# Kernel tuning notes

Hardware: AMD Instinct MI355X
Metric: run time of the kernel (lower is better)

Reference implementation:

```python
import jax, jax.numpy as jnp
import numpy as np

N = 8388608  # flattened batch*seq tokens
C = 2        # binary classification, per source


def setup_inputs() -> dict:
    key = jax.random.key(0)
    k1, k2 = jax.random.split(key)
    x = jax.random.normal(k1, (N, C), dtype=jnp.float32)
    targets = jax.random.randint(k2, (N,), 0, 2, dtype=jnp.int64)
    return {"x": x, "targets": targets}


def reference(x, targets):
    # log-softmax over classes
    logs = jax.nn.log_softmax(x, axis=1)  # [N, C]
    # gather log-prob at the target class per sample
    picked = jnp.take_along_axis(logs, targets[:, None].astype(jnp.int32), axis=1)[:, 0]  # [N]
    is_one = (targets == 1)
    is_zero = (targets == 0)
    n_one = jnp.sum(is_one)
    n_zero = jnp.sum(is_zero)
    sum_one = jnp.sum(jnp.where(is_one, picked, 0.0))
    sum_zero = jnp.sum(jnp.where(is_zero, picked, 0.0))
    # class-conditional mean of -log p; 0 if the class is absent
    r = jnp.where(n_one > 0, -sum_one / jnp.maximum(n_one, 1), 0.0)
    p = jnp.where(n_zero > 0, -sum_zero / jnp.maximum(n_zero, 1), 0.0)
    return p + r
```

## Files before the change

kernel.cpp:

```cpp
#include <hip/hip_runtime.h>

#define BLOCK 256
#define NBLOCKS 2048
#define BLOCK2 256

__global__ __launch_bounds__(BLOCK) void nll_partial(
    const float4* __restrict__ x4,
    const int4* __restrict__ t4,
    float* __restrict__ ps0,
    float* __restrict__ ps1,
    unsigned int* __restrict__ pc1,
    int nquads)
{
    int idx = blockIdx.x * blockDim.x + threadIdx.x;
    int stride = gridDim.x * blockDim.x;

    float s0 = 0.f, s1 = 0.f;
    unsigned int c1 = 0;

    for (int i = idx; i < nquads; i += stride) {
        float4 xa = x4[2 * i];
        float4 xb = x4[2 * i + 1];
        int4   t  = t4[i];

        float a, b, m, lse;

        a = xa.x; b = xa.y;
        m = fmaxf(a, b);
        lse = m + __logf(__expf(a - m) + __expf(b - m));
        s1 += t.x ? (lse - b) : 0.f;
        s0 += t.x ? 0.f : (lse - a);
        c1 += (t.x != 0);

        a = xa.z; b = xa.w;
        m = fmaxf(a, b);
        lse = m + __logf(__expf(a - m) + __expf(b - m));
        s1 += t.y ? (lse - b) : 0.f;
        s0 += t.y ? 0.f : (lse - a);
        c1 += (t.y != 0);

        a = xb.x; b = xb.y;
        m = fmaxf(a, b);
        lse = m + __logf(__expf(a - m) + __expf(b - m));
        s1 += t.z ? (lse - b) : 0.f;
        s0 += t.z ? 0.f : (lse - a);
        c1 += (t.z != 0);

        a = xb.z; b = xb.w;
        m = fmaxf(a, b);
        lse = m + __logf(__expf(a - m) + __expf(b - m));
        s1 += t.w ? (lse - b) : 0.f;
        s0 += t.w ? 0.f : (lse - a);
        c1 += (t.w != 0);
    }

    for (int off = 32; off > 0; off >>= 1) {
        s0 += __shfl_down(s0, off, 64);
        s1 += __shfl_down(s1, off, 64);
        c1 += __shfl_down(c1, off, 64);
    }

    __shared__ float sh0[BLOCK / 64];
    __shared__ float sh1[BLOCK / 64];
    __shared__ unsigned int shc[BLOCK / 64];

    int lane = threadIdx.x & 63;
    int wave = threadIdx.x >> 6;
    if (lane == 0) { sh0[wave] = s0; sh1[wave] = s1; shc[wave] = c1; }
    __syncthreads();

    if (threadIdx.x == 0) {
        float t0 = 0.f, t1 = 0.f;
        unsigned int tc = 0;
        for (int w = 0; w < BLOCK / 64; ++w) { t0 += sh0[w]; t1 += sh1[w]; tc += shc[w]; }
        ps0[blockIdx.x] = t0;
        ps1[blockIdx.x] = t1;
        pc1[blockIdx.x] = tc;
    }
}

__global__ __launch_bounds__(BLOCK2) void nll_finalize(
    const float* __restrict__ ps0,
    const float* __restrict__ ps1,
    const unsigned int* __restrict__ pc1,
    const float* __restrict__ x,
    const int* __restrict__ tg,
    float* __restrict__ out,
    int P, int N, int tail_start)
{
    float s0 = 0.f, s1 = 0.f;
    unsigned int c1 = 0;
    for (int i = threadIdx.x; i < P; i += BLOCK2) {
        s0 += ps0[i];
        s1 += ps1[i];
        c1 += pc1[i];
    }

    for (int off = 32; off > 0; off >>= 1) {
        s0 += __shfl_down(s0, off, 64);
        s1 += __shfl_down(s1, off, 64);
        c1 += __shfl_down(c1, off, 64);
    }

    __shared__ float sh0[BLOCK2 / 64];
    __shared__ float sh1[BLOCK2 / 64];
    __shared__ unsigned int shc[BLOCK2 / 64];

    int lane = threadIdx.x & 63;
    int wave = threadIdx.x >> 6;
    if (lane == 0) { sh0[wave] = s0; sh1[wave] = s1; shc[wave] = c1; }
    __syncthreads();

    if (threadIdx.x == 0) {
        float t0 = 0.f, t1 = 0.f;
        unsigned int tc = 0;
        for (int w = 0; w < BLOCK2 / 64; ++w) { t0 += sh0[w]; t1 += sh1[w]; tc += shc[w]; }
        for (int i = tail_start; i < N; ++i) {
            float a = x[2 * i], b = x[2 * i + 1];
            float m = fmaxf(a, b);
            float lse = m + __logf(__expf(a - m) + __expf(b - m));
            if (tg[i]) { t1 += lse - b; tc++; } else { t0 += lse - a; }
        }
        unsigned int c0 = (unsigned int)N - tc;
        float r = (tc > 0) ? t1 / (float)tc : 0.f;
        float p = (c0 > 0) ? t0 / (float)c0 : 0.f;
        out[0] = p + r;
    }
}

__global__ void nll_atomic(const float4* __restrict__ x4,
                           const int4* __restrict__ t4,
                           float* __restrict__ wsf,
                           unsigned int* __restrict__ wsi,
                           int nquads)
{
    int idx = blockIdx.x * blockDim.x + threadIdx.x;
    int stride = gridDim.x * blockDim.x;
    float s0 = 0.f, s1 = 0.f;
    unsigned int c1 = 0;
    for (int i = idx; i < nquads; i += stride) {
        float4 xa = x4[2 * i];
        float4 xb = x4[2 * i + 1];
        int4   t  = t4[i];
        float a, b, m, lse;
        a = xa.x; b = xa.y; m = fmaxf(a, b);
        lse = m + __logf(__expf(a - m) + __expf(b - m));
        s1 += t.x ? (lse - b) : 0.f; s0 += t.x ? 0.f : (lse - a); c1 += (t.x != 0);
        a = xa.z; b = xa.w; m = fmaxf(a, b);
        lse = m + __logf(__expf(a - m) + __expf(b - m));
        s1 += t.y ? (lse - b) : 0.f; s0 += t.y ? 0.f : (lse - a); c1 += (t.y != 0);
        a = xb.x; b = xb.y; m = fmaxf(a, b);
        lse = m + __logf(__expf(a - m) + __expf(b - m));
        s1 += t.z ? (lse - b) : 0.f; s0 += t.z ? 0.f : (lse - a); c1 += (t.z != 0);
        a = xb.z; b = xb.w; m = fmaxf(a, b);
        lse = m + __logf(__expf(a - m) + __expf(b - m));
        s1 += t.w ? (lse - b) : 0.f; s0 += t.w ? 0.f : (lse - a); c1 += (t.w != 0);
    }
    for (int off = 32; off > 0; off >>= 1) {
        s0 += __shfl_down(s0, off, 64);
        s1 += __shfl_down(s1, off, 64);
        c1 += __shfl_down(c1, off, 64);
    }
    __shared__ float sh0[4]; __shared__ float sh1[4]; __shared__ unsigned int shc[4];
    int lane = threadIdx.x & 63; int wave = threadIdx.x >> 6;
    if (lane == 0) { sh0[wave] = s0; sh1[wave] = s1; shc[wave] = c1; }
    __syncthreads();
    if (threadIdx.x == 0) {
        float t0 = 0.f, t1 = 0.f; unsigned int tc = 0;
        for (int w = 0; w < 4; ++w) { t0 += sh0[w]; t1 += sh1[w]; tc += shc[w]; }
        atomicAdd(&wsf[0], t0); atomicAdd(&wsf[1], t1); atomicAdd(&wsi[0], tc);
    }
}

__global__ void nll_atomic_fin(const float* __restrict__ x,
                               const int* __restrict__ tg,
                               const float* __restrict__ wsf,
                               const unsigned int* __restrict__ wsi,
                               float* __restrict__ out,
                               int N, int tail_start)
{
    float s0 = wsf[0], s1 = wsf[1];
    unsigned int c1 = wsi[0];
    for (int i = tail_start; i < N; ++i) {
        float a = x[2 * i], b = x[2 * i + 1];
        float m = fmaxf(a, b);
        float lse = m + __logf(__expf(a - m) + __expf(b - m));
        if (tg[i]) { s1 += lse - b; c1++; } else { s0 += lse - a; }
    }
    unsigned int c0 = (unsigned int)N - c1;
    float r = (c1 > 0) ? s1 / (float)c1 : 0.f;
    float p = (c0 > 0) ? s0 / (float)c0 : 0.f;
    out[0] = p + r;
}

extern "C" void kernel_launch(void* const* d_in, const int* in_sizes, int n_in,
                              void* d_out, int out_size, void* d_ws, size_t ws_size,
                              hipStream_t stream) {
    const float* x = (const float*)d_in[0];
    const int* tg = (const int*)d_in[1];
    int N = in_sizes[1];
    float* out = (float*)d_out;

    int nquads = N / 4;
    int tail_start = nquads * 4;

    size_t need = (size_t)NBLOCKS * (4 + 4 + 4);
    if (ws_size >= need) {
        float* ps0 = (float*)d_ws;
        float* ps1 = ps0 + NBLOCKS;
        unsigned int* pc1 = (unsigned int*)(ps1 + NBLOCKS);

        nll_partial<<<NBLOCKS, BLOCK, 0, stream>>>(
            (const float4*)x, (const int4*)tg, ps0, ps1, pc1, nquads);
        nll_finalize<<<1, BLOCK2, 0, stream>>>(
            ps0, ps1, pc1, x, tg, out, NBLOCKS, N, tail_start);
    } else {
        float* wsf = (float*)d_ws;
        unsigned int* wsi = (unsigned int*)((char*)d_ws + 8);
        hipMemsetAsync(d_ws, 0, 16, stream);
        nll_atomic<<<256, BLOCK, 0, stream>>>(
            (const float4*)x, (const int4*)tg, wsf, wsi, nquads);
        nll_atomic_fin<<<1, 1, 0, stream>>>(x, tg, wsf, wsi, out, N, tail_start);
    }
}
```

Baseline: 115.8 us.

## Use softplus form, nontemporal loads, and 4x unrolled pair-wise streaming loop

The main kernel now processes two samples per thread per step with a 16-byte x load and an 8-byte target load, unrolled four times across grid strides so more loads are in flight. Loads use nontemporal hints to avoid polluting the cache. The two-class log-softmax is rewritten as softplus of the logit difference, which drops one exp per sample. The narrower target loads halve the per-lane load width compared with the previous int4 access, and the numerics change slightly.

New measurement: 121.4 us. 4.8% more time.

```diff
diff --git a/kernel.cpp b/kernel.cpp
--- a/kernel.cpp
+++ b/kernel.cpp
@@ -4,54 +4,61 @@
 #define NBLOCKS 2048
 #define BLOCK2 256
 
+typedef float v4f __attribute__((ext_vector_type(4)));
+typedef int   v2i __attribute__((ext_vector_type(2)));
+
+__device__ __forceinline__ void acc_pair(v4f xv, v2i tv,
+                                         float& s0, float& s1, unsigned int& c1)
+{
+    {
+        float z = tv[0] ? (xv[0] - xv[1]) : (xv[1] - xv[0]);
+        float l = fmaxf(z, 0.f) + __logf(1.f + __expf(-fabsf(z)));
+        s1 += tv[0] ? l : 0.f;
+        s0 += tv[0] ? 0.f : l;
+        c1 += (tv[0] != 0);
+    }
+    {
+        float z = tv[1] ? (xv[2] - xv[3]) : (xv[3] - xv[2]);
+        float l = fmaxf(z, 0.f) + __logf(1.f + __expf(-fabsf(z)));
+        s1 += tv[1] ? l : 0.f;
+        s0 += tv[1] ? 0.f : l;
+        c1 += (tv[1] != 0);
+    }
+}
+
 __global__ __launch_bounds__(BLOCK) void nll_partial(
-    const float4* __restrict__ x4,
-    const int4* __restrict__ t4,
+    const v4f* __restrict__ xp,
+    const v2i* __restrict__ tp,
     float* __restrict__ ps0,
     float* __restrict__ ps1,
     unsigned int* __restrict__ pc1,
-    int nquads)
-{
-    int idx = blockIdx.x * blockDim.x + threadIdx.x;
-    int stride = gridDim.x * blockDim.x;
+    int npairs)
+{
+    int idx = blockIdx.x * BLOCK + threadIdx.x;
+    int stride = gridDim.x * BLOCK;
 
     float s0 = 0.f, s1 = 0.f;
     unsigned int c1 = 0;
 
-    for (int i = idx; i < nquads; i += stride) {
-        float4 xa = x4[2 * i];
-        float4 xb = x4[2 * i + 1];
-        int4   t  = t4[i];
-
-        float a, b, m, lse;
-
-        a = xa.x; b = xa.y;
-        m = fmaxf(a, b);
-        lse = m + __logf(__expf(a - m) + __expf(b - m));
-        s1 += t.x ? (lse - b) : 0.f;
-        s0 += t.x ? 0.f : (lse - a);
-        c1 += (t.x != 0);
-
-        a = xa.z; b = xa.w;
-        m = fmaxf(a, b);
-        lse = m + __logf(__expf(a - m) + __expf(b - m));
-        s1 += t.y ? (lse - b) : 0.f;
-        s0 += t.y ? 0.f : (lse - a);
-        c1 += (t.y != 0);
-
-        a = xb.x; b = xb.y;
-        m = fmaxf(a, b);
-        lse = m + __logf(__expf(a - m) + __expf(b - m));
-        s1 += t.z ? (lse - b) : 0.f;
-        s0 += t.z ? 0.f : (lse - a);
-        c1 += (t.z != 0);
-
-        a = xb.z; b = xb.w;
-        m = fmaxf(a, b);
-        lse = m + __logf(__expf(a - m) + __expf(b - m));
-        s1 += t.w ? (lse - b) : 0.f;
-        s0 += t.w ? 0.f : (lse - a);
-        c1 += (t.w != 0);
+    int i = idx;
+    for (; i + 3 * stride < npairs; i += 4 * stride) {
+        v4f x0 = __builtin_nontemporal_load(&xp[i]);
+        v4f x1 = __builtin_nontemporal_load(&xp[i + stride]);
+        v4f x2 = __builtin_nontemporal_load(&xp[i + 2 * stride]);
+        v4f x3 = __builtin_nontemporal_load(&xp[i + 3 * stride]);
+        v2i t0 = __builtin_nontemporal_load(&tp[i]);
+        v2i t1 = __builtin_nontemporal_load(&tp[i + stride]);
+        v2i t2 = __builtin_nontemporal_load(&tp[i + 2 * stride]);
+        v2i t3 = __builtin_nontemporal_load(&tp[i + 3 * stride]);
+        acc_pair(x0, t0, s0, s1, c1);
+        acc_pair(x1, t1, s0, s1, c1);
+        acc_pair(x2, t2, s0, s1, c1);
+        acc_pair(x3, t3, s0, s1, c1);
+    }
+    for (; i < npairs; i += stride) {
+        v4f xv = __builtin_nontemporal_load(&xp[i]);
+        v2i tv = __builtin_nontemporal_load(&tp[i]);
+        acc_pair(xv, tv, s0, s1, c1);
     }
 
     for (int off = 32; off > 0; off >>= 1) {
@@ -117,9 +124,9 @@
         for (int w = 0; w < BLOCK2 / 64; ++w) { t0 += sh0[w]; t1 += sh1[w]; tc += shc[w]; }
         for (int i = tail_start; i < N; ++i) {
             float a = x[2 * i], b = x[2 * i + 1];
-            float m = fmaxf(a, b);
-            float lse = m + __logf(__expf(a - m) + __expf(b - m));
-            if (tg[i]) { t1 += lse - b; tc++; } else { t0 += lse - a; }
+            float z = tg[i] ? (a - b) : (b - a);
+            float l = fmaxf(z, 0.f) + __logf(1.f + __expf(-fabsf(z)));
+            if (tg[i]) { t1 += l; tc++; } else { t0 += l; }
         }
         unsigned int c0 = (unsigned int)N - tc;
         float r = (tc > 0) ? t1 / (float)tc : 0.f;
@@ -128,33 +135,20 @@
     }
 }
 
-__global__ void nll_atomic(const float4* __restrict__ x4,
-                           const int4* __restrict__ t4,
+__global__ void nll_atomic(const v4f* __restrict__ xp,
+                           const v2i* __restrict__ tp,
                            float* __restrict__ wsf,
                            unsigned int* __restrict__ wsi,
-                           int nquads)
+                           int npairs)
 {
     int idx = blockIdx.x * blockDim.x + threadIdx.x;
     int stride = gridDim.x * blockDim.x;
     float s0 = 0.f, s1 = 0.f;
     unsigned int c1 = 0;
-    for (int i = idx; i < nquads; i += stride) {
-        float4 xa = x4[2 * i];
-        float4 xb = x4[2 * i + 1];
-        int4   t  = t4[i];
-        float a, b, m, lse;
-        a = xa.x; b = xa.y; m = fmaxf(a, b);
-        lse = m + __logf(__expf(a - m) + __expf(b - m));
-        s1 += t.x ? (lse - b) : 0.f; s0 += t.x ? 0.f : (lse - a); c1 += (t.x != 0);
-        a = xa.z; b = xa.w; m = fmaxf(a, b);
-        lse = m + __logf(__expf(a - m) + __expf(b - m));
-        s1 += t.y ? (lse - b) : 0.f; s0 += t.y ? 0.f : (lse - a); c1 += (t.y != 0);
-        a = xb.x; b = xb.y; m = fmaxf(a, b);
-        lse = m + __logf(__expf(a - m) + __expf(b - m));
-        s1 += t.z ? (lse - b) : 0.f; s0 += t.z ? 0.f : (lse - a); c1 += (t.z != 0);
-        a = xb.z; b = xb.w; m = fmaxf(a, b);
-        lse = m + __logf(__expf(a - m) + __expf(b - m));
-        s1 += t.w ? (lse - b) : 0.f; s0 += t.w ? 0.f : (lse - a); c1 += (t.w != 0);
+    for (int i = idx; i < npairs; i += stride) {
+        v4f xv = xp[i];
+        v2i tv = tp[i];
+        acc_pair(xv, tv, s0, s1, c1);
     }
     for (int off = 32; off > 0; off >>= 1) {
         s0 += __shfl_down(s0, off, 64);
@@ -183,9 +177,9 @@
     unsigned int c1 = wsi[0];
     for (int i = tail_start; i < N; ++i) {
         float a = x[2 * i], b = x[2 * i + 1];
-        float m = fmaxf(a, b);
-        float lse = m + __logf(__expf(a - m) + __expf(b - m));
-        if (tg[i]) { s1 += lse - b; c1++; } else { s0 += lse - a; }
+        float z = tg[i] ? (a - b) : (b - a);
+        float l = fmaxf(z, 0.f) + __logf(1.f + __expf(-fabsf(z)));
+        if (tg[i]) { s1 += l; c1++; } else { s0 += l; }
     }
     unsigned int c0 = (unsigned int)N - c1;
     float r = (c1 > 0) ? s1 / (float)c1 : 0.f;
@@ -201,8 +195,8 @@
     int N = in_sizes[1];
     float* out = (float*)d_out;
 
-    int nquads = N / 4;
-    int tail_start = nquads * 4;
+    int npairs = N / 2;
+    int tail_start = npairs * 2;
 
     size_t need = (size_t)NBLOCKS * (4 + 4 + 4);
     if (ws_size >= need) {
@@ -211,7 +205,7 @@
         unsigned int* pc1 = (unsigned int*)(ps1 + NBLOCKS);
 
         nll_partial<<<NBLOCKS, BLOCK, 0, stream>>>(
-            (const float4*)x, (const int4*)tg, ps0, ps1, pc1, nquads);
+            (const v4f*)x, (const v2i*)tg, ps0, ps1, pc1, npairs);
         nll_finalize<<<1, BLOCK2, 0, stream>>>(
             ps0, ps1, pc1, x, tg, out, NBLOCKS, N, tail_start);
     } else {
@@ -219,7 +213,7 @@
         unsigned int* wsi = (unsigned int*)((char*)d_ws + 8);
         hipMemsetAsync(d_ws, 0, 16, stream);
         nll_atomic<<<256, BLOCK, 0, stream>>>(
-            (const float4*)x, (const int4*)tg, wsf, wsi, nquads);
+            (const v4f*)x, (const v2i*)tg, wsf, wsi, npairs);
         nll_atomic_fin<<<1, 1, 0, stream>>>(x, tg, wsf, wsi, out, N, tail_start);
     }
 }
```
